# Optimization experiments

Hardware: AMD Instinct MI355X
Metric: run time of the kernel (lower is better)

## Reference

```python
import jax, jax.numpy as jnp
import numpy as np

TOPK = 4


def setup_inputs() -> dict:
    key = jax.random.key(0)
    ks = jax.random.split(key, 9)
    B, T, D = 4, 2048, 1024
    E, H = 32, 128          # routed experts, per-expert hidden
    HS = H * TOPK           # shared expert hidden = 512
    s = lambda k, shape, fan: jax.random.normal(k, shape, dtype=jnp.float32) / np.sqrt(fan)
    return {
        "x": jax.random.normal(ks[0], (B, T, D), dtype=jnp.float32),
        "router_w": s(ks[1], (E, D), D),
        "router_bias": jnp.zeros((E,), dtype=jnp.float32),
        "gate_w": s(ks[2], (E, H, D), D),
        "up_w": s(ks[3], (E, H, D), D),
        "down_w": s(ks[4], (E, D, H), H),
        "sgate_w": s(ks[5], (HS, D), D),
        "sup_w": s(ks[6], (HS, D), D),
        "sdown_w": s(ks[7], (D, HS), HS),
    }


def reference(x, router_w, router_bias, gate_w, up_w, down_w, sgate_w, sup_w, sdown_w):
    B, T, D = x.shape
    flat = x.reshape(B * T, D)                                   # [N, D]
    # Router (fp32 logits + persistent bias buffer)
    logits = flat.astype(jnp.float32) @ router_w.T + router_bias  # [N, E]
    scores = jax.nn.softmax(logits, axis=-1)
    topk_scores, topk_idx = jax.lax.top_k(scores, TOPK)          # [N, K]
    topk_scores = topk_scores / jnp.clip(
        topk_scores.sum(axis=-1, keepdims=True), 1e-12, None)
    # Dense all-expert SwiGLU (matches torch.stack over experts)
    h = jax.nn.silu(jnp.einsum("nd,ehd->neh", flat, gate_w)) \
        * jnp.einsum("nd,ehd->neh", flat, up_w)                  # [N, E, H]
    expert_out = jnp.einsum("neh,edh->ned", h, down_w)           # [N, E, D]
    # Gather top-k expert outputs, scale, combine
    sel = jnp.take_along_axis(expert_out, topk_idx[:, :, None], axis=1)  # [N, K, D]
    out = (sel * topk_scores.astype(flat.dtype)[:, :, None]).sum(axis=1)  # [N, D]
    # Always-on shared expert (SwiGLU)
    out = out + (jax.nn.silu(flat @ sgate_w.T) * (flat @ sup_w.T)) @ sdown_w.T
    return out.reshape(B, T, D)
```

## Files before the change

kernel.cpp:

```cpp
#include <hip/hip_runtime.h>
#include <hip/hip_bf16.h>
#include <math.h>

#define N_TOK 8192
#define DIM   1024
#define E_R   32
#define H_E   128
#define HS    512
#define TOPK  4
#define RKS   8
#define RKL   (DIM / RKS)
#define MAXSLOT 34816

typedef __bf16 bf16;
typedef __bf16 bf16x8 __attribute__((ext_vector_type(8)));
typedef float  floatx4 __attribute__((ext_vector_type(4)));

#define MFMA16(a,b,c) __builtin_amdgcn_mfma_f32_16x16x32_bf16(a,b,c,0,0,0)

__device__ __forceinline__ void gl_lds16(const bf16* g, bf16* l) {
    __builtin_amdgcn_global_load_lds(
        (const __attribute__((address_space(1))) void*)g,
        (__attribute__((address_space(3))) void*)l, 16, 0, 0);
}

__global__ __launch_bounds__(256)
void cvt_all(const float* __restrict__ x, const float* __restrict__ g,
             const float* __restrict__ u, const float* __restrict__ d,
             const float* __restrict__ sg, const float* __restrict__ su,
             const float* __restrict__ sd,
             bf16* __restrict__ xb, bf16* __restrict__ gb, bf16* __restrict__ ub,
             bf16* __restrict__ db, bf16* __restrict__ sgb, bf16* __restrict__ sub,
             bf16* __restrict__ sdb) {
    int b = blockIdx.x;
    const float* s; bf16* o; int lb;
    if      (b < 4096)  { s = x;  o = xb;  lb = b; }
    else if (b < 6144)  { s = g;  o = gb;  lb = b - 4096; }
    else if (b < 8192)  { s = u;  o = ub;  lb = b - 6144; }
    else if (b < 10240) { s = d;  o = db;  lb = b - 8192; }
    else if (b < 10496) { s = sg; o = sgb; lb = b - 10240; }
    else if (b < 10752) { s = su; o = sub; lb = b - 10496; }
    else                { s = sd; o = sdb; lb = b - 10752; }
    size_t i = (size_t)lb * 2048 + threadIdx.x * 8;
    float4 v0 = *(const float4*)(s + i);
    float4 v1 = *(const float4*)(s + i + 4);
    bf16x8 r = {(bf16)v0.x,(bf16)v0.y,(bf16)v0.z,(bf16)v0.w,
                (bf16)v1.x,(bf16)v1.y,(bf16)v1.z,(bf16)v1.w};
    *(bf16x8*)(o + i) = r;
}

__global__ __launch_bounds__(256)
void router_gemm(const float* __restrict__ x, const float* __restrict__ rw,
                 float* __restrict__ partial) {
    __shared__ float Xs[64 * 132];
    __shared__ float Wt[128 * 32];
    int tid = threadIdx.x;
    int t0  = blockIdx.x * 64;
    int kb  = blockIdx.y * RKL;

#pragma unroll
    for (int j = 0; j < 8; ++j) {
        int flat = j * 1024 + tid * 4;
        int row = flat >> 7, col = flat & 127;
        float4 v = *(const float4*)(x + (size_t)(t0 + row) * DIM + kb + col);
        *(float4*)(&Xs[row * 132 + col]) = v;
    }
    {
        int e = tid >> 3, kq = (tid & 7) * 16;
        const float* wp = rw + (size_t)e * DIM + kb + kq;
#pragma unroll
        for (int i = 0; i < 16; i += 4) {
            float4 v = *(const float4*)(wp + i);
            Wt[(kq + i + 0) * 32 + e] = v.x;
            Wt[(kq + i + 1) * 32 + e] = v.y;
            Wt[(kq + i + 2) * 32 + e] = v.z;
            Wt[(kq + i + 3) * 32 + e] = v.w;
        }
    }
    __syncthreads();

    int eg = tid & 7, tg = tid >> 3;
    float acc[2][4] = {{0.f}};
#pragma unroll 4
    for (int k = 0; k < RKL; k += 4) {
        float4 xa0 = *(const float4*)(&Xs[(tg * 2 + 0) * 132 + k]);
        float4 xa1 = *(const float4*)(&Xs[(tg * 2 + 1) * 132 + k]);
#pragma unroll
        for (int kk = 0; kk < 4; ++kk) {
            float4 w = *(const float4*)(&Wt[(k + kk) * 32 + eg * 4]);
            float x0 = (&xa0.x)[kk], x1 = (&xa1.x)[kk];
            acc[0][0] += x0 * w.x; acc[0][1] += x0 * w.y;
            acc[0][2] += x0 * w.z; acc[0][3] += x0 * w.w;
            acc[1][0] += x1 * w.x; acc[1][1] += x1 * w.y;
            acc[1][2] += x1 * w.z; acc[1][3] += x1 * w.w;
        }
    }
#pragma unroll
    for (int t = 0; t < 2; ++t) {
        floatx4 v = { acc[t][0], acc[t][1], acc[t][2], acc[t][3] };
        *(floatx4*)(&partial[((size_t)blockIdx.y * N_TOK + t0 + tg * 2 + t) * 32 + eg * 4]) = v;
    }
}

__global__ __launch_bounds__(256)
void router_fin(const float* __restrict__ partial, const float* __restrict__ rb,
                int* __restrict__ counts, int* __restrict__ tlist,
                float* __restrict__ slist, int* __restrict__ tok2slot) {
    __shared__ int lcnt[E_R];
    __shared__ int gbase[E_R];
    int tid = threadIdx.x;
    int n = blockIdx.x * 256 + tid;
    if (tid < E_R) lcnt[tid] = 0;
    __syncthreads();

    float lg[E_R];
#pragma unroll
    for (int e4 = 0; e4 < E_R; e4 += 4) {
        floatx4 s = {0.f, 0.f, 0.f, 0.f};
#pragma unroll
        for (int ks = 0; ks < RKS; ++ks)
            s += *(const floatx4*)(&partial[((size_t)ks * N_TOK + n) * 32 + e4]);
        lg[e4 + 0] = s[0] + rb[e4 + 0];
        lg[e4 + 1] = s[1] + rb[e4 + 1];
        lg[e4 + 2] = s[2] + rb[e4 + 2];
        lg[e4 + 3] = s[3] + rb[e4 + 3];
    }
    float mx = -1e30f;
#pragma unroll
    for (int e = 0; e < E_R; ++e) mx = fmaxf(mx, lg[e]);
    float se = 0.f;
#pragma unroll
    for (int e = 0; e < E_R; ++e) { float v = __expf(lg[e] - mx); lg[e] = v; se += v; }
    float inv = 1.f / se;

    unsigned usedMask = 0;
    int idx[TOPK]; float pv[TOPK]; int lpos[TOPK]; float psum = 0.f;
    for (int k = 0; k < TOPK; ++k) {
        float best = -1.f; int bi = 0;
        for (int e = 0; e < E_R; ++e)
            if (!((usedMask >> e) & 1) && lg[e] > best) { best = lg[e]; bi = e; }
        usedMask |= 1u << bi;
        idx[k] = bi; pv[k] = best * inv; psum += pv[k];
    }
    float norm = 1.f / fmaxf(psum, 1e-12f);
#pragma unroll
    for (int k = 0; k < TOPK; ++k)
        lpos[k] = atomicAdd(&lcnt[idx[k]], 1);
    __syncthreads();
    if (tid < E_R) gbase[tid] = atomicAdd(&counts[tid], lcnt[tid]);
    __syncthreads();
#pragma unroll
    for (int k = 0; k < TOPK; ++k) {
        int e = idx[k];
        int pos = gbase[e] + lpos[k];
        tlist[(size_t)e * N_TOK + pos] = n;
        slist[(size_t)e * N_TOK + pos] = pv[k] * norm;
        tok2slot[(size_t)n * 4 + k] = (e << 16) | pos;
    }
}

__global__ void wq_build(const int* __restrict__ counts, int* __restrict__ items,
                         int* __restrict__ nitems, int* __restrict__ expbase) {
    if (threadIdx.x == 0) {
        int n = 0, base = 0;
        for (int e = 0; e < E_R; ++e) {
            int c = counts[e];
            expbase[e] = base;
            int nt = (c + 63) >> 6;
            for (int t = 0; t < nt; ++t)
                items[n++] = (e << 24) | (t << 16) | (base + t * 64);
            base += nt * 64;
        }
        *nitems = n;
    }
}

__global__ __launch_bounds__(256, 3)
void phase1(const bf16* __restrict__ xb, const bf16* __restrict__ wg,
            const bf16* __restrict__ wu, const bf16* __restrict__ sg,
            const bf16* __restrict__ su, const int* __restrict__ counts,
            const int* __restrict__ tlist, const int* __restrict__ items,
            const int* __restrict__ nitems,
            bf16* __restrict__ Hg, bf16* __restrict__ Hs) {
    __shared__ __align__(16) bf16 As[2 * 64 * 32];
    __shared__ __align__(16) bf16 Bs[2 * 256 * 32];

    int b = blockIdx.x;
    const bf16 *gptr, *uptr;
    bf16* hout; int hstride;
    int e, lbase, cnt = 0;
    if (b < 512) {
        int c = b >> 7, t = b & 127;
        gptr = sg + (size_t)c * H_E * DIM;
        uptr = su + (size_t)c * H_E * DIM;
        hout = Hs + (size_t)t * 64 * HS + c * H_E;
        hstride = HS;
        lbase = t * 64;
        e = -1;
    } else {
        int rbk = b - 512;
        if (rbk >= *nitems) return;
        int it = items[rbk];
        e = it >> 24; int t = (it >> 16) & 0xff; int rowbase = it & 0xffff;
        gptr = wg + (size_t)e * H_E * DIM;
        uptr = wu + (size_t)e * H_E * DIM;
        hout = Hg + (size_t)rowbase * H_E;
        hstride = H_E;
        cnt = counts[e];
        lbase = t * 64;
    }

    int tid = threadIdx.x;
    int r = tid >> 2;
    int chunk = (((tid & 3) ^ ((tid >> 3) & 3))) * 8;
    int tok;
    if (e < 0) tok = lbase + r;
    else { int li = lbase + r; if (li >= cnt) li = cnt - 1; tok = tlist[(size_t)e * N_TOK + li]; }
    const bf16* aSrc = xb + (size_t)tok * DIM + chunk;
    const bf16* gSrc = gptr + (size_t)r * DIM + chunk;
    const bf16* uSrc = uptr + (size_t)r * DIM + chunk;

    int w = tid >> 6, lane = tid & 63, m = lane & 15, quad = lane >> 4;
    int quadx = quad ^ ((m >> 1) & 3);

    floatx4 aG[4][2] = {{{0}}};
    floatx4 aU[4][2] = {{{0}}};

    #define P1_STAGE(buf, k0)                                                  \
        do {                                                                   \
            bf16* aD = As + (buf) * 2048 + tid * 8;                            \
            bf16* bD = Bs + (buf) * 8192 + tid * 8;                            \
            gl_lds16(aSrc + (k0), aD);                                         \
            gl_lds16(gSrc + (k0), bD);                                         \
            gl_lds16(gSrc + 64 * DIM + (k0), bD + 2048);                       \
            gl_lds16(uSrc + (k0), bD + 4096);                                  \
            gl_lds16(uSrc + 64 * DIM + (k0), bD + 6144);                       \
        } while (0)

    P1_STAGE(0, 0);
    __syncthreads();

    int cur = 0;
    for (int k0 = 0; k0 < DIM; k0 += 32) {
        if (k0 + 32 < DIM) P1_STAGE(cur ^ 1, k0 + 32);
        const bf16* Ab = As + cur * 2048;
        const bf16* Bb = Bs + cur * 8192;
        bf16x8 a[4], bg[2], bu[2];
#pragma unroll
        for (int mg = 0; mg < 4; ++mg)
            a[mg] = *(const bf16x8*)(Ab + (mg * 16 + m) * 32 + quadx * 8);
#pragma unroll
        for (int j = 0; j < 2; ++j) {
            bg[j] = *(const bf16x8*)(Bb + (w * 32 + j * 16 + m) * 32 + quadx * 8);
            bu[j] = *(const bf16x8*)(Bb + (128 + w * 32 + j * 16 + m) * 32 + quadx * 8);
        }
#pragma unroll
        for (int j = 0; j < 2; ++j)
#pragma unroll
            for (int mg = 0; mg < 4; ++mg) {
                aG[mg][j] = MFMA16(a[mg], bg[j], aG[mg][j]);
                aU[mg][j] = MFMA16(a[mg], bu[j], aU[mg][j]);
            }
        __syncthreads();
        cur ^= 1;
    }
    #undef P1_STAGE

#pragma unroll
    for (int mg = 0; mg < 4; ++mg)
#pragma unroll
        for (int j = 0; j < 2; ++j)
#pragma unroll
            for (int r4 = 0; r4 < 4; ++r4) {
                float gv = aG[mg][j][r4], uv = aU[mg][j][r4];
                float h = gv / (1.f + __expf(-gv)) * uv;
                hout[(size_t)(mg * 16 + quad * 4 + r4) * hstride + w * 32 + j * 16 + m] = (bf16)h;
            }
}

__global__ __launch_bounds__(256, 3)
void phase2(const bf16* __restrict__ Hg, const bf16* __restrict__ wd,
            const int* __restrict__ counts, const float* __restrict__ slist,
            const int* __restrict__ items, const int* __restrict__ nitems,
            bf16* __restrict__ Od) {
    __shared__ __align__(16) bf16 As[2 * 64 * 32];
    __shared__ __align__(16) bf16 Bs[2 * 256 * 32];
    __shared__ float ssc[64];

    int rbk = blockIdx.x;
    if (rbk >= *nitems) return;
    int it = items[rbk];
    int e = it >> 24, t = (it >> 16) & 0xff, rowbase = it & 0xffff;
    int n0 = blockIdx.y * 256;
    int cnt = counts[e];

    int tid = threadIdx.x;
    if (tid < 64) {
        int li = t * 64 + tid;
        ssc[tid] = (li < cnt) ? slist[(size_t)e * N_TOK + li] : 0.f;
    }

    int r = tid >> 2;
    int chunk = (((tid & 3) ^ ((tid >> 3) & 3))) * 8;
    const bf16* aSrc = Hg + (size_t)(rowbase + r) * H_E + chunk;
    const bf16* bSrc = wd + (size_t)e * DIM * H_E + (size_t)(n0 + r) * H_E + chunk;

    int w = tid >> 6, lane = tid & 63, m = lane & 15, quad = lane >> 4;
    int quadx = quad ^ ((m >> 1) & 3);
    floatx4 acc[4][4] = {{{0}}};

    #define P2_STAGE(buf, k0)                                                  \
        do {                                                                   \
            bf16* aD = As + (buf) * 2048 + tid * 8;                            \
            bf16* bD = Bs + (buf) * 8192 + tid * 8;                            \
            gl_lds16(aSrc + (k0), aD);                                         \
            _Pragma("unroll")                                                  \
            for (int p = 0; p < 4; ++p)                                        \
                gl_lds16(bSrc + (size_t)p * 64 * H_E + (k0), bD + p * 2048);   \
        } while (0)

    P2_STAGE(0, 0);
    __syncthreads();

    int cur = 0;
    for (int k0 = 0; k0 < H_E; k0 += 32) {
        if (k0 + 32 < H_E) P2_STAGE(cur ^ 1, k0 + 32);
        const bf16* Ab = As + cur * 2048;
        const bf16* Bb = Bs + cur * 8192;
        bf16x8 a[4], bb[4];
#pragma unroll
        for (int mg = 0; mg < 4; ++mg)
            a[mg] = *(const bf16x8*)(Ab + (mg * 16 + m) * 32 + quadx * 8);
#pragma unroll
        for (int ng = 0; ng < 4; ++ng)
            bb[ng] = *(const bf16x8*)(Bb + (w * 64 + ng * 16 + m) * 32 + quadx * 8);
#pragma unroll
        for (int ng = 0; ng < 4; ++ng)
#pragma unroll
            for (int mg = 0; mg < 4; ++mg)
                acc[mg][ng] = MFMA16(a[mg], bb[ng], acc[mg][ng]);
        __syncthreads();
        cur ^= 1;
    }
    #undef P2_STAGE

#pragma unroll
    for (int mg = 0; mg < 4; ++mg)
#pragma unroll
        for (int r4 = 0; r4 < 4; ++r4) {
            int row = mg * 16 + quad * 4 + r4;
            float sc = ssc[row];
            bf16* op = Od + (size_t)(rowbase + row) * DIM + n0 + w * 64 + m;
#pragma unroll
            for (int ng = 0; ng < 4; ++ng)
                op[ng * 16] = (bf16)(acc[mg][ng][r4] * sc);
        }
}

__global__ __launch_bounds__(256, 3)
void shared_down(const bf16* __restrict__ Hs, const bf16* __restrict__ sd,
                 const bf16* __restrict__ Od, const int* __restrict__ tok2slot,
                 const int* __restrict__ expbase, float* __restrict__ out) {
    __shared__ __align__(16) bf16 As[2 * 64 * 32];
    __shared__ __align__(16) bf16 Bs[2 * 256 * 32];
    __shared__ int srow[64][4];

    int t0 = blockIdx.x * 64;
    int n0 = blockIdx.y * 256;
    int tid = threadIdx.x;

    if (tid < 64) {
        const int* t2s = tok2slot + (size_t)(t0 + tid) * 4;
#pragma unroll
        for (int k = 0; k < 4; ++k) {
            int v = t2s[k];
            srow[tid][k] = expbase[v >> 16] + (v & 0xffff);
        }
    }

    int r = tid >> 2;
    int chunk = (((tid & 3) ^ ((tid >> 3) & 3))) * 8;
    const bf16* aSrc = Hs + (size_t)(t0 + r) * HS + chunk;
    const bf16* bSrc = sd + (size_t)(n0 + r) * HS + chunk;

    int w = tid >> 6, lane = tid & 63, m = lane & 15, quad = lane >> 4;
    int quadx = quad ^ ((m >> 1) & 3);
    floatx4 acc[4][4] = {{{0}}};

    #define SD_STAGE(buf, k0)                                                  \
        do {                                                                   \
            bf16* aD = As + (buf) * 2048 + tid * 8;                            \
            bf16* bD = Bs + (buf) * 8192 + tid * 8;                            \
            gl_lds16(aSrc + (k0), aD);                                         \
            _Pragma("unroll")                                                  \
            for (int p = 0; p < 4; ++p)                                        \
                gl_lds16(bSrc + (size_t)p * 64 * HS + (k0), bD + p * 2048);    \
        } while (0)

    SD_STAGE(0, 0);
    __syncthreads();

    int cur = 0;
    for (int k0 = 0; k0 < HS; k0 += 32) {
        if (k0 + 32 < HS) SD_STAGE(cur ^ 1, k0 + 32);
        const bf16* Ab = As + cur * 2048;
        const bf16* Bb = Bs + cur * 8192;
        bf16x8 a[4], bb[4];
#pragma unroll
        for (int mg = 0; mg < 4; ++mg)
            a[mg] = *(const bf16x8*)(Ab + (mg * 16 + m) * 32 + quadx * 8);
#pragma unroll
        for (int ng = 0; ng < 4; ++ng)
            bb[ng] = *(const bf16x8*)(Bb + (w * 64 + ng * 16 + m) * 32 + quadx * 8);
#pragma unroll
        for (int ng = 0; ng < 4; ++ng)
#pragma unroll
            for (int mg = 0; mg < 4; ++mg)
                acc[mg][ng] = MFMA16(a[mg], bb[ng], acc[mg][ng]);
        __syncthreads();
        cur ^= 1;
    }
    #undef SD_STAGE

#pragma unroll
    for (int mg = 0; mg < 4; ++mg)
#pragma unroll
        for (int r4 = 0; r4 < 4; ++r4) {
            int rl = mg * 16 + quad * 4 + r4;
            size_t r0 = (size_t)srow[rl][0] * DIM;
            size_t r1 = (size_t)srow[rl][1] * DIM;
            size_t r2 = (size_t)srow[rl][2] * DIM;
            size_t r3 = (size_t)srow[rl][3] * DIM;
            float* op = out + (size_t)(t0 + rl) * DIM + n0 + w * 64 + m;
#pragma unroll
            for (int ng = 0; ng < 4; ++ng) {
                int col = n0 + w * 64 + ng * 16 + m;
                float v = acc[mg][ng][r4]
                        + (float)Od[r0 + col] + (float)Od[r1 + col]
                        + (float)Od[r2 + col] + (float)Od[r3 + col];
                op[ng * 16] = v;
            }
        }
}

extern "C" void kernel_launch(void* const* d_in, const int* in_sizes, int n_in,
                              void* d_out, int out_size, void* d_ws, size_t ws_size,
                              hipStream_t stream) {
    (void)in_sizes; (void)n_in; (void)out_size; (void)ws_size;
    const float* x   = (const float*)d_in[0];
    const float* rw  = (const float*)d_in[1];
    const float* rb  = (const float*)d_in[2];
    const float* gw  = (const float*)d_in[3];
    const float* uw  = (const float*)d_in[4];
    const float* dw  = (const float*)d_in[5];
    const float* sgw = (const float*)d_in[6];
    const float* suw = (const float*)d_in[7];
    const float* sdw = (const float*)d_in[8];
    float* out = (float*)d_out;

    char* ws = (char*)d_ws;
    size_t o = 0;
    bf16* xb  = (bf16*)(ws + o); o += (size_t)N_TOK * DIM * 2;
    bf16* wgb = (bf16*)(ws + o); o += (size_t)E_R * H_E * DIM * 2;
    bf16* wub = (bf16*)(ws + o); o += (size_t)E_R * H_E * DIM * 2;
    bf16* wdb = (bf16*)(ws + o); o += (size_t)E_R * DIM * H_E * 2;
    bf16* sgb = (bf16*)(ws + o); o += (size_t)HS * DIM * 2;
    bf16* sub = (bf16*)(ws + o); o += (size_t)HS * DIM * 2;
    bf16* sdb = (bf16*)(ws + o); o += (size_t)DIM * HS * 2;
    bf16* Hg  = (bf16*)(ws + o); o += (size_t)MAXSLOT * H_E * 2;
    bf16* Hs  = (bf16*)(ws + o); o += (size_t)N_TOK * HS * 2;
    bf16* Od  = (bf16*)(ws + o); o += (size_t)MAXSLOT * DIM * 2;
    float* partial = (float*)(ws + o); o += (size_t)RKS * N_TOK * 32 * 4;
    int*   counts = (int*)(ws + o);   o += 256;
    int*   tlist  = (int*)(ws + o);   o += (size_t)E_R * N_TOK * 4;
    float* slist  = (float*)(ws + o); o += (size_t)E_R * N_TOK * 4;
    int*   tok2slot = (int*)(ws + o); o += (size_t)N_TOK * 4 * 4;
    int*   items  = (int*)(ws + o);   o += 4096;
    int*   nitems = (int*)(ws + o);   o += 64;
    int*   expbase = (int*)(ws + o);  o += 256;

    hipMemsetAsync(counts, 0, E_R * sizeof(int), stream);

    router_gemm<<<dim3(N_TOK / 64, RKS), 256, 0, stream>>>(x, rw, partial);
    router_fin<<<N_TOK / 256, 256, 0, stream>>>(partial, rb, counts, tlist, slist,
                                                tok2slot);
    cvt_all<<<11008, 256, 0, stream>>>(x, gw, uw, dw, sgw, suw, sdw,
                                       xb, wgb, wub, wdb, sgb, sub, sdb);
    wq_build<<<1, 64, 0, stream>>>(counts, items, nitems, expbase);
    phase1<<<1056, 256, 0, stream>>>(xb, wgb, wub, sgb, sub, counts, tlist,
                                     items, nitems, Hg, Hs);
    phase2<<<dim3(544, 4), 256, 0, stream>>>(Hg, wdb, counts, slist,
                                             items, nitems, Od);
    shared_down<<<dim3(N_TOK / 64, 4), 256, 0, stream>>>(Hs, sdb, Od, tok2slot,
                                                         expbase, out);
}
```

Baseline: 309.0 us.

## Triple-buffer LDS pipeline with vmcnt-based barriers in MoE GEMM kernels

Converts the double-buffered global-to-LDS staging in phase1, phase2 and shared_down into a three-stage ring buffer. Two tiles are prefetched before the loop, and each iteration waits with s_waitcnt vmcnt(5) plus a barrier, so the next tile's loads stay in flight while the current tile is computed. The aim is to hide global load latency better and drop one barrier per iteration. In exchange it uses 1.5x the LDS, and occupancy hints drop from 3 to 2 blocks per CU. The barrier only waits for the older loads, which relies on each stage issuing exactly 5 loads per thread.

Result: no change. 314.1 us (+1.7%).

```diff
diff --git a/kernel.cpp b/kernel.cpp
--- a/kernel.cpp
+++ b/kernel.cpp
@@ -23,6 +23,10 @@
         (const __attribute__((address_space(1))) void*)g,
         (__attribute__((address_space(3))) void*)l, 16, 0, 0);
 }
+
+#define PIPE_BAR(n) asm volatile("s_waitcnt lgkmcnt(0)\n\t"                   \
+                                 "s_waitcnt vmcnt(" #n ")\n\t"                \
+                                 "s_barrier" ::: "memory")
 
 __global__ __launch_bounds__(256)
 void cvt_all(const float* __restrict__ x, const float* __restrict__ g,
@@ -175,15 +179,15 @@
     }
 }
 
-__global__ __launch_bounds__(256, 3)
+__global__ __launch_bounds__(256, 2)
 void phase1(const bf16* __restrict__ xb, const bf16* __restrict__ wg,
             const bf16* __restrict__ wu, const bf16* __restrict__ sg,
             const bf16* __restrict__ su, const int* __restrict__ counts,
             const int* __restrict__ tlist, const int* __restrict__ items,
             const int* __restrict__ nitems,
             bf16* __restrict__ Hg, bf16* __restrict__ Hs) {
-    __shared__ __align__(16) bf16 As[2 * 64 * 32];
-    __shared__ __align__(16) bf16 Bs[2 * 256 * 32];
+    __shared__ __align__(16) bf16 As[3 * 64 * 32];
+    __shared__ __align__(16) bf16 Bs[3 * 256 * 32];
 
     int b = blockIdx.x;
     const bf16 *gptr, *uptr;
@@ -238,11 +242,11 @@
         } while (0)
 
     P1_STAGE(0, 0);
-    __syncthreads();
-
-    int cur = 0;
-    for (int k0 = 0; k0 < DIM; k0 += 32) {
-        if (k0 + 32 < DIM) P1_STAGE(cur ^ 1, k0 + 32);
+    P1_STAGE(1, 32);
+
+    for (int t = 0; t < 32; ++t) {
+        if (t < 31) PIPE_BAR(5); else PIPE_BAR(0);
+        int cur = t % 3;
         const bf16* Ab = As + cur * 2048;
         const bf16* Bb = Bs + cur * 8192;
         bf16x8 a[4], bg[2], bu[2];
@@ -261,8 +265,7 @@
                 aG[mg][j] = MFMA16(a[mg], bg[j], aG[mg][j]);
                 aU[mg][j] = MFMA16(a[mg], bu[j], aU[mg][j]);
             }
-        __syncthreads();
-        cur ^= 1;
+        if (t + 2 < 32) P1_STAGE((t + 2) % 3, (t + 2) * 32);
     }
     #undef P1_STAGE
 
@@ -278,13 +281,13 @@
             }
 }
 
-__global__ __launch_bounds__(256, 3)
+__global__ __launch_bounds__(256, 2)
 void phase2(const bf16* __restrict__ Hg, const bf16* __restrict__ wd,
             const int* __restrict__ counts, const float* __restrict__ slist,
             const int* __restrict__ items, const int* __restrict__ nitems,
             bf16* __restrict__ Od) {
-    __shared__ __align__(16) bf16 As[2 * 64 * 32];
-    __shared__ __align__(16) bf16 Bs[2 * 256 * 32];
+    __shared__ __align__(16) bf16 As[3 * 64 * 32];
+    __shared__ __align__(16) bf16 Bs[3 * 256 * 32];
     __shared__ float ssc[64];
 
     int rbk = blockIdx.x;
@@ -320,11 +323,11 @@
         } while (0)
 
     P2_STAGE(0, 0);
-    __syncthreads();
-
-    int cur = 0;
-    for (int k0 = 0; k0 < H_E; k0 += 32) {
-        if (k0 + 32 < H_E) P2_STAGE(cur ^ 1, k0 + 32);
+    P2_STAGE(1, 32);
+
+    for (int tt = 0; tt < 4; ++tt) {
+        if (tt < 3) PIPE_BAR(5); else PIPE_BAR(0);
+        int cur = tt % 3;
         const bf16* Ab = As + cur * 2048;
         const bf16* Bb = Bs + cur * 8192;
         bf16x8 a[4], bb[4];
@@ -339,8 +342,7 @@
 #pragma unroll
             for (int mg = 0; mg < 4; ++mg)
                 acc[mg][ng] = MFMA16(a[mg], bb[ng], acc[mg][ng]);
-        __syncthreads();
-        cur ^= 1;
+        if (tt + 2 < 4) P2_STAGE((tt + 2) % 3, (tt + 2) * 32);
     }
     #undef P2_STAGE
 
@@ -357,12 +359,12 @@
         }
 }
 
-__global__ __launch_bounds__(256, 3)
+__global__ __launch_bounds__(256, 2)
 void shared_down(const bf16* __restrict__ Hs, const bf16* __restrict__ sd,
                  const bf16* __restrict__ Od, const int* __restrict__ tok2slot,
                  const int* __restrict__ expbase, float* __restrict__ out) {
-    __shared__ __align__(16) bf16 As[2 * 64 * 32];
-    __shared__ __align__(16) bf16 Bs[2 * 256 * 32];
+    __shared__ __align__(16) bf16 As[3 * 64 * 32];
+    __shared__ __align__(16) bf16 Bs[3 * 256 * 32];
     __shared__ int srow[64][4];
 
     int t0 = blockIdx.x * 64;
@@ -398,11 +400,11 @@
         } while (0)
 
     SD_STAGE(0, 0);
-    __syncthreads();
-
-    int cur = 0;
-    for (int k0 = 0; k0 < HS; k0 += 32) {
-        if (k0 + 32 < HS) SD_STAGE(cur ^ 1, k0 + 32);
+    SD_STAGE(1, 32);
+
+    for (int tt = 0; tt < 16; ++tt) {
+        if (tt < 15) PIPE_BAR(5); else PIPE_BAR(0);
+        int cur = tt % 3;
         const bf16* Ab = As + cur * 2048;
         const bf16* Bb = Bs + cur * 8192;
         bf16x8 a[4], bb[4];
@@ -417,8 +419,7 @@
 #pragma unroll
             for (int mg = 0; mg < 4; ++mg)
                 acc[mg][ng] = MFMA16(a[mg], bb[ng], acc[mg][ng]);
-        __syncthreads();
-        cur ^= 1;
+        if (tt + 2 < 16) SD_STAGE((tt + 2) % 3, (tt + 2) * 32);
     }
     #undef SD_STAGE
 
```
